# Optimization experiments

Measured on AMD Instinct MI355X. Metric: run time of the kernel, lower is better.

The kernel has to match this reference:

```python
import jax, jax.numpy as jnp
import numpy as np

B, L, D, V = 2048, 32, 256, 100000  # batch, sentence length, embed dim, vocab
KW = 3  # kernel_width (forced to 3 by the module's shape arithmetic)


def conv_h(x, w, b):
    """1-channel conv over the seq axis, kernel (3,1), pad 2 -> length L+2. x:(B,L,D), w:(3,)."""
    xp = jnp.pad(x, ((0, 0), (2, 2), (0, 0)))
    L_out = x.shape[1] + 2
    out = w[0] * xp[:, 0:L_out] + w[1] * xp[:, 1:L_out + 1] + w[2] * xp[:, 2:L_out + 2]
    return out + b


def avgpool3(x):
    """avg_pool2d kernel (3,1) stride 1 along seq axis. (B,L+2,D) -> (B,L,D)."""
    return (x[:, :-2] + x[:, 1:-1] + x[:, 2:]) / 3.0


def conv3d_21(x, w, b):
    """Conv3d kernel (2,3,1), pad (0,2,0). x:(B,2,L,D), w:(2,3) -> (B,L+2,D)."""
    xp = jnp.pad(x, ((0, 0), (0, 0), (2, 2), (0, 0)))
    L_out = x.shape[2] + 2
    out = jnp.zeros((x.shape[0], L_out, x.shape[3]), dtype=x.dtype)
    for d0 in range(2):
        for k in range(3):
            out = out + w[d0, k] * xp[:, d0, k:k + L_out]
    return out + b


def euclid_attention(a, b):
    """A[k,i,j] = 1/(1 + ||a[k,i]-b[k,j]||_2), computed via the matmul cdist trick."""
    a2 = jnp.sum(a * a, axis=-1)  # (B,La)
    b2 = jnp.sum(b * b, axis=-1)  # (B,Lb)
    d2 = a2[:, :, None] + b2[:, None, :] - 2.0 * jnp.einsum('bid,bjd->bij', a, b)
    d = jnp.sqrt(jnp.maximum(d2, 0.0))
    return 1.0 / (1.0 + d)


def setup_inputs() -> dict:
    key = jax.random.key(0)
    ks = jax.random.split(key, 16)
    inp = {
        'sentence1': jax.random.randint(ks[0], (B, L), 0, V),
        'sentence2': jax.random.randint(ks[1], (B, L), 0, V),
        'embed': jax.random.normal(ks[2], (V, D), dtype=jnp.float32) * 0.05,
        'c1w': jax.random.normal(ks[3], (KW,), dtype=jnp.float32) * 0.3,
        'c1b': jax.random.normal(ks[4], (), dtype=jnp.float32) * 0.05,
        'c2w': jax.random.normal(ks[5], (KW,), dtype=jnp.float32) * 0.3,
        'c2b': jax.random.normal(ks[6], (), dtype=jnp.float32) * 0.05,
        'c3w': jax.random.normal(ks[7], (2, KW), dtype=jnp.float32) * 0.3,
        'c3b': jax.random.normal(ks[8], (), dtype=jnp.float32) * 0.05,
        'W0': jax.random.normal(ks[9], (L, D), dtype=jnp.float32),
        'W1': jax.random.normal(ks[10], (L, D), dtype=jnp.float32),
        'fw1': jax.random.normal(ks[11], (2 * D, 64), dtype=jnp.float32) * 0.05,
        'fb1': jnp.zeros((64,), dtype=jnp.float32),
        'fw2': jax.random.normal(ks[12], (64, 2), dtype=jnp.float32) * 0.1,
        'fb2': jnp.zeros((2,), dtype=jnp.float32),
    }
    return inp


def reference(sentence1, sentence2, embed, c1w, c1b, c2w, c2b, c3w, c3b, W0, W1, fw1, fb1, fw2, fb2):
    e1 = embed[sentence1]                      # (B,L,D)
    e2 = embed[sentence2]
    rep1 = avgpool3(conv_h(e1, c1w, c1b))      # (B,L,D)
    rep2 = avgpool3(conv_h(e2, c1w, c1b))
    A1 = euclid_attention(rep1, rep2)          # (B,L,L)
    att1 = jnp.einsum('bij,jd->bid', A1, W0)   # (B,L,D)
    att2 = jnp.einsum('bij,jd->bid', A1, W1)
    c1 = conv3d_21(jnp.stack([rep1, att1], axis=1), c3w, c3b)  # (B,L+2,D)
    c2 = conv3d_21(jnp.stack([rep2, att2], axis=1), c3w, c3b)
    A2 = euclid_attention(c1, c2)              # (B,L+2,L+2)
    col = jnp.sum(A2, axis=2)                  # (B,L+2)
    row = jnp.sum(A2, axis=1)
    ca1 = avgpool3(c1 * col[:, :, None])       # (B,L,D)
    ca2 = avgpool3(c2 * row[:, :, None])
    v1 = jnp.mean(conv_h(ca1, c2w, c2b), axis=1)  # (B,D)
    v2 = jnp.mean(conv_h(ca2, c2w, c2b), axis=1)
    h = jnp.tanh(jnp.concatenate([v1, v2], axis=1) @ fw1 + fb1)
    logits = h @ fw2 + fb2                     # (B,2)
    return jax.nn.softmax(logits, axis=0)      # faithful: original Softmax(dim=0)
```

## Files before the change

### kernel.cpp

```cpp
#include <hip/hip_runtime.h>
#include <math.h>

#define NB 2048
#define LL 32
#define DD 256
#define LP 34
#define SRH 264
#define SA 35

typedef unsigned short u16;
typedef short bf8 __attribute__((ext_vector_type(8)));
typedef float f32x4 __attribute__((ext_vector_type(4)));
typedef float vf2 __attribute__((ext_vector_type(2)));

__device__ __forceinline__ float bfu(u16 h) { return __uint_as_float(((unsigned)h) << 16); }
__device__ __forceinline__ u16 f2bf(float f) {
    unsigned u = __float_as_uint(f);
    u += 0x7fffu + ((u >> 16) & 1u);
    return (u16)(u >> 16);
}
__device__ __forceinline__ unsigned cvt_pk_bf(float lo, float hi) {
    unsigned r;
    asm("v_cvt_pk_bf16_f32 %0, %1, %2" : "=v"(r) : "v"(lo), "v"(hi));
    return r;
}

__device__ __forceinline__ f32x4 gram8(const u16* __restrict__ A, const u16* __restrict__ B) {
    f32x4 acc = {0.f, 0.f, 0.f, 0.f};
    #pragma unroll
    for (int ks = 0; ks < 8; ++ks) {
        const bf8 a = *(const bf8*)(A + ks * 32);
        const bf8 b = *(const bf8*)(B + ks * 32);
        acc = __builtin_amdgcn_mfma_f32_16x16x32_bf16(a, b, acc, 0, 0, 0);
    }
    return acc;
}

__device__ static const signed char TB2[8][4] = {
    {0,0,1,0}, {0,0,1,16}, {0,16,1,0}, {0,16,1,16},
    {0,0,0,0}, {0,16,0,16}, {1,0,1,0}, {1,16,1,16}};

__device__ static const signed char TB5[15][4] = {
    {0,0,0,0}, {0,16,0,16}, {0,18,0,18}, {1,0,1,0}, {1,16,1,16}, {1,18,1,18},
    {0,0,1,0},  {0,0,1,16},  {0,0,1,18},
    {0,16,1,0}, {0,16,1,16}, {0,16,1,18},
    {0,18,1,0}, {0,18,1,16}, {0,18,1,18}};

__global__ __launch_bounds__(256)
void pack_w(const float* __restrict__ W0, const float* __restrict__ W1, u16* __restrict__ wp)
{
    const int t = blockIdx.x * 256 + threadIdx.x;
    const int lane = t & 63, nt = (t >> 6) & 15, wsel = t >> 10;
    const float* W = wsel ? W1 : W0;
    const int col = nt * 16 + (lane & 15);
    const int k0 = (lane >> 4) * 8;
    unsigned d[4];
    #pragma unroll
    for (int q = 0; q < 4; ++q) {
        const u16 lo = f2bf(W[(size_t)(k0 + 2 * q) * DD + col]);
        const u16 hi = f2bf(W[(size_t)(k0 + 2 * q + 1) * DD + col]);
        d[q] = (unsigned)lo | ((unsigned)hi << 16);
    }
    uint4 u; u.x = d[0]; u.y = d[1]; u.z = d[2]; u.w = d[3];
    ((uint4*)wp)[t] = u;
}

__global__ __attribute__((amdgpu_flat_work_group_size(256, 256), amdgpu_waves_per_eu(4, 4)))
void abcnn_fused(const int* __restrict__ s1, const int* __restrict__ s2,
                 const float* __restrict__ embed,
                 const float* __restrict__ c1w, const float* __restrict__ c1b,
                 const float* __restrict__ c2w, const float* __restrict__ c2b,
                 const float* __restrict__ c3w, const float* __restrict__ c3b,
                 const float* __restrict__ fw1, const float* __restrict__ fb1,
                 const float* __restrict__ fw2, const float* __restrict__ fb2,
                 const u16* __restrict__ wpack, float* __restrict__ lgts)
{
    __shared__ __align__(16) u16 RC[2][LP][SRH];
    __shared__ float AU[LP * SA];
    __shared__ float nrm[2][LP];

    const int b    = blockIdx.x;
    const int tid  = threadIdx.x;
    const int lane = tid & 63;
    const int wv   = tid >> 6;
    const int c15  = lane & 15;
    const int q4x  = (lane >> 4) * 4;
    const int ko   = (lane >> 4) * 8;

    {
        const float w0 = c1w[0], w1 = c1w[1], w2 = c1w[2], bb = c1b[0];
        const float gm2 = w0 * (1.f/3.f);
        const float gm1 = (w0 + w1) * (1.f/3.f);
        const float g0  = (w0 + w1 + w2) * (1.f/3.f);
        const float gp1 = (w1 + w2) * (1.f/3.f);
        const float gp2 = w2 * (1.f/3.f);
        const int s  = __builtin_amdgcn_readfirstlane(tid >> 7);
        const int dp = tid & 127;
        const int* sent = (s ? s2 : s1) + b * LL;
        int sv[LL];
        #pragma unroll
        for (int j = 0; j < LL; ++j) sv[j] = sent[j];
        #pragma unroll
        for (int half = 0; half < 2; ++half) {
            const int j0 = half * 16;
            vf2 x[20];
            #pragma unroll
            for (int i = 0; i < 20; ++i) {
                const int rr = j0 - 2 + i;
                if (rr >= 0 && rr < LL)
                    x[i] = *(const vf2*)(embed + (size_t)sv[rr] * DD + 2 * dp);
                else
                    x[i] = (vf2){0.f, 0.f};
            }
            #pragma unroll
            for (int j = 0; j < 16; ++j) {
                vf2 acc = {bb, bb};
                acc += gm2 * x[j];
                acc += gm1 * x[j + 1];
                acc += g0  * x[j + 2];
                acc += gp1 * x[j + 3];
                acc += gp2 * x[j + 4];
                *(unsigned*)&RC[s][j0 + j][2 * dp] = cvt_pk_bf(acc.x, acc.y);
            }
        }
    }
    __syncthreads();

    {
        f32x4 h2[2];
        __builtin_amdgcn_s_setprio(1);
        #pragma unroll
        for (int k = 0; k < 2; ++k) {
            const int t  = wv * 2 + k;
            const int sa = TB2[t][0], oa = TB2[t][1], sb = TB2[t][2], ob = TB2[t][3];
            const f32x4 G = gram8(&RC[sa][oa + c15][ko], &RC[sb][ob + c15][ko]);
            h2[k] = G;
            if (t >= 4 && (c15 >> 2) == (lane >> 4)) {
                const int r = c15 & 3;
                const float dv = (r == 0) ? G[0] : (r == 1) ? G[1] : (r == 2) ? G[2] : G[3];
                nrm[sa][oa + c15] = dv;
            }
        }
        __builtin_amdgcn_s_setprio(0);
        __syncthreads();
        #pragma unroll
        for (int k = 0; k < 2; ++k) {
            const int t = wv * 2 + k;
            if (t < 4) {
                const int oa = TB2[t][1], ob = TB2[t][3];
                const f32x4 G = h2[k];
                #pragma unroll
                for (int r = 0; r < 4; ++r) {
                    const int i = oa + q4x + r, j = ob + c15;
                    const float d2 = nrm[0][i] + nrm[1][j] - 2.f * G[r];
                    AU[i * SA + j] = 1.f / (1.f + sqrtf(fmaxf(d2, 0.f)));
                }
            }
        }
    }
    __syncthreads();

    {
        const float cw10 = c3w[3], cw11 = c3w[4], cw12 = c3w[5];
        const float cw00 = c3w[0], cw01 = c3w[1], cw02 = c3w[2], cb3 = c3b[0];
        bf8 afr[3];
        #pragma unroll
        for (int rq = 0; rq < 3; ++rq) {
            const int ro = (rq == 0) ? 0 : (rq == 1) ? 16 : 18;
            const int i = ro + c15;
            unsigned pk[4];
            #pragma unroll
            for (int p = 0; p < 4; ++p) {
                float e[2];
                #pragma unroll
                for (int hh = 0; hh < 2; ++hh) {
                    const int m = ko + 2 * p + hh;
                    float acc = 0.f;
                    if (i >= 2)           acc += cw10 * AU[(i - 2) * SA + m];
                    if (i >= 1 && i < 33) acc += cw11 * AU[(i - 1) * SA + m];
                    if (i < 32)           acc += cw12 * AU[i * SA + m];
                    e[hh] = acc;
                }
                pk[p] = cvt_pk_bf(e[0], e[1]);
            }
            afr[rq] = *(bf8*)&pk[0];
        }
        for (int wsel = 0; wsel < 2; ++wsel) {
            f32x4 acc[12];
            __builtin_amdgcn_s_setprio(1);
            #pragma unroll
            for (int k = 0; k < 12; ++k) {
                const int rq = k >> 2;
                const int ro = (rq == 0) ? 0 : (rq == 1) ? 16 : 18;
                const int n  = wv + 4 * (k & 3);
                const bf8 w = *(const bf8*)(wpack + (size_t)((wsel * 16 + n) * 64 + lane) * 8);
                const f32x4 z = {0.f, 0.f, 0.f, 0.f};
                f32x4 d = __builtin_amdgcn_mfma_f32_16x16x32_bf16(afr[rq], w, z, 0, 0, 0);
                const int dcol = n * 16 + c15;
                const int i0 = ro + q4x;
                float tt[6];
                #pragma unroll
                for (int q2 = 0; q2 < 6; ++q2) {
                    const int rr = i0 - 2 + q2;
                    tt[q2] = (rr >= 0 && rr < LL) ? bfu(RC[wsel][rr][dcol]) : 0.f;
                }
                #pragma unroll
                for (int r = 0; r < 4; ++r)
                    d[r] += cb3 + cw00 * tt[r] + cw01 * tt[r + 1] + cw02 * tt[r + 2];
                acc[k] = d;
            }
            __builtin_amdgcn_s_setprio(0);
            __syncthreads();
            #pragma unroll
            for (int k = 0; k < 12; ++k) {
                const int rq = k >> 2;
                const int ro = (rq == 0) ? 0 : (rq == 1) ? 16 : 18;
                const int n  = wv + 4 * (k & 3);
                const int dcol = n * 16 + c15;
                const int i0 = ro + q4x;
                const unsigned p01 = cvt_pk_bf(acc[k][0], acc[k][1]);
                const unsigned p23 = cvt_pk_bf(acc[k][2], acc[k][3]);
                RC[wsel][i0    ][dcol] = (u16)p01;
                RC[wsel][i0 + 1][dcol] = (u16)(p01 >> 16);
                RC[wsel][i0 + 2][dcol] = (u16)p23;
                RC[wsel][i0 + 3][dcol] = (u16)(p23 >> 16);
            }
            __syncthreads();
        }
    }

    {
        f32x4 h5[4];
        __builtin_amdgcn_s_setprio(1);
        #pragma unroll
        for (int k = 0; k < 4; ++k) {
            const int t = wv + 4 * k;
            if (t < 15) {
                const int sa = TB5[t][0], oa = TB5[t][1], sb = TB5[t][2], ob = TB5[t][3];
                const f32x4 G = gram8(&RC[sa][oa + c15][ko], &RC[sb][ob + c15][ko]);
                h5[k] = G;
                if (t < 6 && (c15 >> 2) == (lane >> 4)) {
                    const int r = c15 & 3;
                    const float dv = (r == 0) ? G[0] : (r == 1) ? G[1] : (r == 2) ? G[2] : G[3];
                    nrm[sa][oa + c15] = dv;
                }
            }
        }
        __builtin_amdgcn_s_setprio(0);
        __syncthreads();
        #pragma unroll
        for (int k = 0; k < 4; ++k) {
            const int t = wv + 4 * k;
            if (t >= 6 && t < 15) {
                const int oa = TB5[t][1], ob = TB5[t][3];
                const f32x4 G = h5[k];
                #pragma unroll
                for (int r = 0; r < 4; ++r) {
                    const int i = oa + q4x + r, j = ob + c15;
                    const float d2 = nrm[0][i] + nrm[1][j] - 2.f * G[r];
                    AU[i * SA + j] = 1.f / (1.f + sqrtf(fmaxf(d2, 0.f)));
                }
            }
        }
    }
    __syncthreads();

    {
        const float S2 = c2w[0] + c2w[1] + c2w[2];
        const float sc = S2 * (1.f / 102.f);
        float p6 = 0.f;
        if (tid < 68) {
            const bool isCol = tid < 34;
            const int p = isCol ? tid : tid - 34;
            float ssum = 0.f;
            for (int q = 0; q < LP; ++q) ssum += AU[isCol ? (p * SA + q) : (q * SA + p)];
            const float cnt = (p == 0 || p == 33) ? 1.f : ((p == 1 || p == 32) ? 2.f : 3.f);
            p6 = ssum * cnt * sc;
        }
        __syncthreads();
        if (tid < 68) AU[tid] = p6;
    }
    __syncthreads();

    {
        const float cb2 = c2b[0];
        float v1 = cb2, v2 = cb2;
        #pragma unroll
        for (int p = 0; p < LP; ++p) {
            v1 += AU[p]      * bfu(RC[0][p][tid]);
            v2 += AU[34 + p] * bfu(RC[1][p][tid]);
        }
        AU[68 + tid]       = v1;
        AU[68 + 256 + tid] = v2;
    }
    __syncthreads();

    {
        const int u = tid & 63, sg = tid >> 6;
        const float* vv = &AU[68];
        const float* fp = fw1 + (size_t)(sg * 128) * 64 + u;
        float part = 0.f;
        for (int t = 0; t < 128; ++t) part += vv[sg * 128 + t] * fp[(size_t)t * 64];
        AU[580 + tid] = part;
    }
    __syncthreads();
    if (tid < 64) {
        const float hsum = AU[580 + tid] + AU[644 + tid] + AU[708 + tid] + AU[772 + tid] + fb1[tid];
        AU[836 + tid] = tanhf(hsum);
    }
    __syncthreads();
    if (tid < 2) {
        float lg = fb2[tid];
        for (int u2 = 0; u2 < 64; ++u2) lg += AU[836 + u2] * fw2[u2 * 2 + tid];
        lgts[tid * NB + b] = lg;
    }
}

__global__ __launch_bounds__(1024)
void softmax_dim0(const float* __restrict__ lgts, float* __restrict__ out)
{
    __shared__ float red[17];
    const int tid = threadIdx.x;
    for (int c = 0; c < 2; ++c) {
        const float x0 = lgts[c * NB + tid];
        const float x1 = lgts[c * NB + 1024 + tid];
        float m = fmaxf(x0, x1);
        #pragma unroll
        for (int off = 32; off >= 1; off >>= 1) m = fmaxf(m, __shfl_xor(m, off));
        if ((tid & 63) == 0) red[tid >> 6] = m;
        __syncthreads();
        if (tid == 0) { float t = red[0]; for (int i = 1; i < 16; ++i) t = fmaxf(t, red[i]); red[16] = t; }
        __syncthreads();
        m = red[16];
        const float e0 = expf(x0 - m), e1 = expf(x1 - m);
        float s = e0 + e1;
        #pragma unroll
        for (int off = 32; off >= 1; off >>= 1) s += __shfl_xor(s, off);
        if ((tid & 63) == 0) red[tid >> 6] = s;
        __syncthreads();
        if (tid == 0) { float t = 0.f; for (int i = 0; i < 16; ++i) t += red[i]; red[16] = t; }
        __syncthreads();
        const float inv = 1.f / red[16];
        out[(size_t)tid * 2 + c]          = e0 * inv;
        out[(size_t)(1024 + tid) * 2 + c] = e1 * inv;
        __syncthreads();
    }
}

extern "C" void kernel_launch(void* const* d_in, const int* in_sizes, int n_in,
                              void* d_out, int out_size, void* d_ws, size_t ws_size,
                              hipStream_t stream)
{
    (void)in_sizes; (void)n_in; (void)out_size; (void)ws_size;
    const int*   s1  = (const int*)  d_in[0];
    const int*   s2  = (const int*)  d_in[1];
    const float* emb = (const float*)d_in[2];
    const float* c1w = (const float*)d_in[3];
    const float* c1b = (const float*)d_in[4];
    const float* c2w = (const float*)d_in[5];
    const float* c2b = (const float*)d_in[6];
    const float* c3w = (const float*)d_in[7];
    const float* c3b = (const float*)d_in[8];
    const float* fw1 = (const float*)d_in[11];
    const float* fb1 = (const float*)d_in[12];
    const float* fw2 = (const float*)d_in[13];
    const float* fb2 = (const float*)d_in[14];
    const float* W0  = (const float*)d_in[9];
    const float* W1  = (const float*)d_in[10];
    u16*   wpack = (u16*)d_ws;
    float* lgts  = (float*)((char*)d_ws + 32768);
    float* out   = (float*)d_out;

    pack_w<<<dim3(8), dim3(256), 0, stream>>>(W0, W1, wpack);
    abcnn_fused<<<dim3(NB), dim3(256), 0, stream>>>(s1, s2, emb, c1w, c1b, c2w, c2b,
                                                    c3w, c3b, fw1, fb1, fw2, fb2,
                                                    wpack, lgts);
    softmax_dim0<<<dim3(1), dim3(1024), 0, stream>>>(lgts, out);
}
```

Baseline: 78.07 us.

## Update conv3d output in place per wave to drop block barriers

Each wave now adds the MFMA attention result to its own columns of the rep tile right away and writes the bf16 result back into RC. It walks the row groups in reverse order so that every row is read before it is overwritten. This removes the 12-entry accumulator array and the two __syncthreads per wsel iteration, keeping a single barrier at the end, and should cut register pressure and barrier stalls. The A-fragment build now packs with a software f2bf per element instead of the packed convert, and the launch attribute is rewritten as __launch_bounds__(256,4).

Result: faster. 66.57 us (-14.7%).

```diff
diff --git a/kernel.cpp b/kernel.cpp
--- a/kernel.cpp
+++ b/kernel.cpp
@@ -65,7 +65,7 @@
     ((uint4*)wp)[t] = u;
 }
 
-__global__ __attribute__((amdgpu_flat_work_group_size(256, 256), amdgpu_waves_per_eu(4, 4)))
+__global__ __launch_bounds__(256, 4)
 void abcnn_fused(const int* __restrict__ s1, const int* __restrict__ s2,
                  const float* __restrict__ embed,
                  const float* __restrict__ c1w, const float* __restrict__ c1b,
@@ -168,66 +168,59 @@
         for (int rq = 0; rq < 3; ++rq) {
             const int ro = (rq == 0) ? 0 : (rq == 1) ? 16 : 18;
             const int i = ro + c15;
-            unsigned pk[4];
+            bf8 af;
             #pragma unroll
-            for (int p = 0; p < 4; ++p) {
-                float e[2];
+            for (int j = 0; j < 8; ++j) {
+                const int m = ko + j;
+                float acc = 0.f;
+                if (i >= 2)           acc += cw10 * AU[(i - 2) * SA + m];
+                if (i >= 1 && i < 33) acc += cw11 * AU[(i - 1) * SA + m];
+                if (i < 32)           acc += cw12 * AU[i * SA + m];
+                af[j] = (short)f2bf(acc);
+            }
+            afr[rq] = af;
+        }
+        __builtin_amdgcn_s_setprio(1);
+        #pragma unroll
+        for (int wsel = 0; wsel < 2; ++wsel) {
+            #pragma unroll
+            for (int nidx = 0; nidx < 4; ++nidx) {
+                const int n = wv + 4 * nidx;
+                const int dcol = n * 16 + c15;
+                const bf8 w = *(const bf8*)(wpack + (size_t)((wsel * 16 + n) * 64 + lane) * 8);
                 #pragma unroll
-                for (int hh = 0; hh < 2; ++hh) {
-                    const int m = ko + 2 * p + hh;
-                    float acc = 0.f;
-                    if (i >= 2)           acc += cw10 * AU[(i - 2) * SA + m];
-                    if (i >= 1 && i < 33) acc += cw11 * AU[(i - 1) * SA + m];
-                    if (i < 32)           acc += cw12 * AU[i * SA + m];
-                    e[hh] = acc;
+                for (int rqd = 0; rqd < 3; ++rqd) {
+                    const int rq = 2 - rqd;
+                    const int ro = (rq == 0) ? 0 : (rq == 1) ? 16 : 18;
+                    const int i0 = ro + q4x;
+                    const f32x4 z = {0.f, 0.f, 0.f, 0.f};
+                    f32x4 d4 = __builtin_amdgcn_mfma_f32_16x16x32_bf16(afr[rq], w, z, 0, 0, 0);
+                    float tt[6];
+                    #pragma unroll
+                    for (int q2 = 0; q2 < 6; ++q2) {
+                        const int rr = i0 - 2 + q2;
+                        tt[q2] = (rr >= 0 && rr < LL) ? bfu(RC[wsel][rr][dcol]) : 0.f;
+                    }
+                    #pragma unroll
+                    for (int r = 0; r < 4; ++r)
+                        d4[r] += cb3 + cw00 * tt[r] + cw01 * tt[r + 1] + cw02 * tt[r + 2];
+                    const unsigned p01 = cvt_pk_bf(d4[0], d4[1]);
+                    const unsigned p23 = cvt_pk_bf(d4[2], d4[3]);
+                    if (rq < 2) {
+                        RC[wsel][i0    ][dcol] = (u16)p01;
+                        RC[wsel][i0 + 1][dcol] = (u16)(p01 >> 16);
+                        RC[wsel][i0 + 2][dcol] = (u16)p23;
+                        RC[wsel][i0 + 3][dcol] = (u16)(p23 >> 16);
+                    } else if (q4x == 12) {
+                        RC[wsel][32][dcol] = (u16)p23;
+                        RC[wsel][33][dcol] = (u16)(p23 >> 16);
+                    }
                 }
-                pk[p] = cvt_pk_bf(e[0], e[1]);
-            }
-            afr[rq] = *(bf8*)&pk[0];
-        }
-        for (int wsel = 0; wsel < 2; ++wsel) {
-            f32x4 acc[12];
-            __builtin_amdgcn_s_setprio(1);
-            #pragma unroll
-            for (int k = 0; k < 12; ++k) {
-                const int rq = k >> 2;
-                const int ro = (rq == 0) ? 0 : (rq == 1) ? 16 : 18;
-                const int n  = wv + 4 * (k & 3);
-                const bf8 w = *(const bf8*)(wpack + (size_t)((wsel * 16 + n) * 64 + lane) * 8);
-                const f32x4 z = {0.f, 0.f, 0.f, 0.f};
-                f32x4 d = __builtin_amdgcn_mfma_f32_16x16x32_bf16(afr[rq], w, z, 0, 0, 0);
-                const int dcol = n * 16 + c15;
-                const int i0 = ro + q4x;
-                float tt[6];
-                #pragma unroll
-                for (int q2 = 0; q2 < 6; ++q2) {
-                    const int rr = i0 - 2 + q2;
-                    tt[q2] = (rr >= 0 && rr < LL) ? bfu(RC[wsel][rr][dcol]) : 0.f;
-                }
-                #pragma unroll
-                for (int r = 0; r < 4; ++r)
-                    d[r] += cb3 + cw00 * tt[r] + cw01 * tt[r + 1] + cw02 * tt[r + 2];
-                acc[k] = d;
-            }
-            __builtin_amdgcn_s_setprio(0);
-            __syncthreads();
-            #pragma unroll
-            for (int k = 0; k < 12; ++k) {
-                const int rq = k >> 2;
-                const int ro = (rq == 0) ? 0 : (rq == 1) ? 16 : 18;
-                const int n  = wv + 4 * (k & 3);
-                const int dcol = n * 16 + c15;
-                const int i0 = ro + q4x;
-                const unsigned p01 = cvt_pk_bf(acc[k][0], acc[k][1]);
-                const unsigned p23 = cvt_pk_bf(acc[k][2], acc[k][3]);
-                RC[wsel][i0    ][dcol] = (u16)p01;
-                RC[wsel][i0 + 1][dcol] = (u16)(p01 >> 16);
-                RC[wsel][i0 + 2][dcol] = (u16)p23;
-                RC[wsel][i0 + 3][dcol] = (u16)(p23 >> 16);
-            }
-            __syncthreads();
-        }
-    }
+            }
+        }
+        __builtin_amdgcn_s_setprio(0);
+    }
+    __syncthreads();
 
     {
         f32x4 h5[4];
```
